# Performance work log

Hardware: AMD Instinct MI355X
Metric: run time of the kernel (lower is better)

The kernel has to match this reference:

```python
import jax, jax.numpy as jnp
import numpy as np

TEMPERATURE = 0.1
EPS = 1e-8  # torch CosineSimilarity eps


def _l2_normalize(x):
    # torch cosine sim: x / max(||x||, eps)
    n = jnp.sqrt(jnp.sum(x * x, axis=1, keepdims=True))
    return x / jnp.maximum(n, EPS)


def _pairwise_softmax(zx, zy):
    # cosine similarity matrix [N, N]: sim[i, j] = cos(zx[i], zy[j])
    sim = _l2_normalize(zx) @ _l2_normalize(zy).T  # [N, N]
    # softmax over dim=1 (columns) after temperature scaling
    return jax.nn.softmax(sim / TEMPERATURE, axis=1)


def _kl_div_mean(log_p, q):
    # torch F.kl_div(input=log_p, target=q, reduction='mean'):
    # mean over ALL elements of q * (log(q) - log_p)
    return jnp.mean(q * (jnp.log(q) - log_p))


def setup_inputs() -> dict:
    key = jax.random.key(0)
    k1, k2, k3, k4 = jax.random.split(key, 4)
    N, D = 4096, 768
    return {
        "zxs": jax.random.normal(k1, (N, D), dtype=jnp.float32),
        "zys": jax.random.normal(k2, (N, D), dtype=jnp.float32),
        "zxt": jax.random.normal(k3, (N, D), dtype=jnp.float32),
        "zyt": jax.random.normal(k4, (N, D), dtype=jnp.float32),
    }


def reference(zxs, zys, zxt, zyt):
    sim_s = _pairwise_softmax(zxs, zys)  # [N, N]
    sim_t = _pairwise_softmax(zxt, zyt)  # [N, N]
    loss_s = _kl_div_mean(jnp.log(sim_s), jax.lax.stop_gradient(sim_t))
    loss_t = _kl_div_mean(jnp.log(sim_t), jax.lax.stop_gradient(sim_s))
    return (loss_s, loss_t)
```

## Files before the change

### kernel.cpp

```cpp
#include <hip/hip_runtime.h>
#include <hip/hip_bf16.h>

#define N 4096
#define D 768
#define NC 6

typedef float f32x4 __attribute__((ext_vector_type(4)));
typedef int v8i __attribute__((ext_vector_type(8)));

typedef __attribute__((address_space(3))) unsigned int as3_uint;
typedef const __attribute__((address_space(1))) unsigned int as1_uint;

__device__ __forceinline__ void gload16(const void* g, void* l) {
    __builtin_amdgcn_global_load_lds((as1_uint*)g, (as3_uint*)l, 16, 0, 0);
}


__global__ __launch_bounds__(256) void norm4(const float* __restrict__ x0,
                                             const float* __restrict__ x1,
                                             const float* __restrict__ x2,
                                             const float* __restrict__ x3,
                                             unsigned char* __restrict__ o) {
    int a = blockIdx.y;
    const float* x = (a == 0) ? x0 : (a == 1) ? x1 : (a == 2) ? x2 : x3;
    unsigned char* out = o + (size_t)a * N * D;
    int i0 = blockIdx.x * 32;
    __shared__ __align__(16) unsigned char tile[24576];
    int t = threadIdx.x, lane = t & 63, w = t >> 6;

    for (int rr = 0; rr < 8; ++rr) {
        int R = i0 + w * 8 + rr;
        const f32x4* xr = (const f32x4*)(x + (size_t)R * D);
        f32x4 v0 = xr[lane * 2], v1 = xr[lane * 2 + 1];
        f32x4 v2 = {}, v3 = {};
        if (lane < 32) { v2 = xr[128 + lane * 2]; v3 = xr[128 + lane * 2 + 1]; }
        float ss = v0[0]*v0[0] + v0[1]*v0[1] + v0[2]*v0[2] + v0[3]*v0[3]
                 + v1[0]*v1[0] + v1[1]*v1[1] + v1[2]*v1[2] + v1[3]*v1[3]
                 + v2[0]*v2[0] + v2[1]*v2[1] + v2[2]*v2[2] + v2[3]*v2[3]
                 + v3[0]*v3[0] + v3[1]*v3[1] + v3[2]*v3[2] + v3[3]*v3[3];
        #pragma unroll
        for (int m = 1; m < 64; m <<= 1) ss += __shfl_xor(ss, m);
        float s = 1.0f / fmaxf(sqrtf(ss), 1e-8f);

        int lrg = (R >> 4) & 1;
        {
            unsigned int wlo = __builtin_amdgcn_cvt_pk_fp8_f32(v0[0]*s, v0[1]*s, 0, false) & 0xffff;
            unsigned int whi = __builtin_amdgcn_cvt_pk_fp8_f32(v0[2]*s, v0[3]*s, 0, false) & 0xffff;
            unsigned int w0 = wlo | (whi << 16);
            wlo = __builtin_amdgcn_cvt_pk_fp8_f32(v1[0]*s, v1[1]*s, 0, false) & 0xffff;
            whi = __builtin_amdgcn_cvt_pk_fp8_f32(v1[2]*s, v1[3]*s, 0, false) & 0xffff;
            unsigned int w1 = wlo | (whi << 16);
            int g = lane;
            int off = (lrg * 6 + (g >> 4)) * 2048 + ((g >> 1) & 1) * 1024
                    + ((R & 15) + 16 * ((g & 15) >> 2)) * 16 + (g & 1) * 8;
            *(uint2*)(tile + off) = make_uint2(w0, w1);
        }
        if (lane < 32) {
            unsigned int wlo = __builtin_amdgcn_cvt_pk_fp8_f32(v2[0]*s, v2[1]*s, 0, false) & 0xffff;
            unsigned int whi = __builtin_amdgcn_cvt_pk_fp8_f32(v2[2]*s, v2[3]*s, 0, false) & 0xffff;
            unsigned int w0 = wlo | (whi << 16);
            wlo = __builtin_amdgcn_cvt_pk_fp8_f32(v3[0]*s, v3[1]*s, 0, false) & 0xffff;
            whi = __builtin_amdgcn_cvt_pk_fp8_f32(v3[2]*s, v3[3]*s, 0, false) & 0xffff;
            unsigned int w1 = wlo | (whi << 16);
            int g = 64 + lane;
            int off = (lrg * 6 + (g >> 4)) * 2048 + ((g >> 1) & 1) * 1024
                    + ((R & 15) + 16 * ((g & 15) >> 2)) * 16 + (g & 1) * 8;
            *(uint2*)(tile + off) = make_uint2(w0, w1);
        }
    }
    __syncthreads();
    unsigned char* dst = out + (size_t)(i0 >> 5) * 24576;
    #pragma unroll
    for (int i = 0; i < 6; ++i)
        ((int4*)dst)[t + i * 256] = ((const int4*)tile)[t + i * 256];
}

__device__ __forceinline__ void gemm_pass(const unsigned char* __restrict__ A,
                                          const unsigned char* __restrict__ B,
                                          char* smem, int ib, int jb, int t,
                                          f32x4 (&acc)[4][4]) {
    const int lane = t & 63, w = t >> 6;
    const int wm = w >> 1, wn = w & 1;

    const unsigned char* gA = A + (size_t)((ib * 8 + 2 * w) * 6) * 2048 + lane * 16;
    const unsigned char* gB = B + (size_t)((jb * 8 + 2 * w) * 6) * 2048 + lane * 16;
    char* cur = smem;
    char* nxt = smem + 32768;
    const int sd = w * 4096 + lane * 16;

    #define ISSUE(dst, c)  do {                                                  \
        const unsigned char* _a = gA + (c) * 2048;                               \
        gload16(_a,         (dst) + sd);                                         \
        gload16(_a + 1024,  (dst) + sd + 1024);                                  \
        gload16(_a + 12288, (dst) + sd + 2048);                                  \
        gload16(_a + 13312, (dst) + sd + 3072);                                  \
        const unsigned char* _b = gB + (c) * 2048;                               \
        gload16(_b,         (dst) + 16384 + sd);                                 \
        gload16(_b + 1024,  (dst) + 16384 + sd + 1024);                          \
        gload16(_b + 12288, (dst) + 16384 + sd + 2048);                          \
        gload16(_b + 13312, (dst) + 16384 + sd + 3072);                          \
    } while (0)

    ISSUE(cur, 0);

    #pragma unroll 1
    for (int c = 0; c < NC; ++c) {
        if (c < NC - 1) {
            ISSUE(nxt, c + 1);
            asm volatile("s_waitcnt vmcnt(8)" ::: "memory");
        } else {
            asm volatile("s_waitcnt vmcnt(0)" ::: "memory");
        }
        __builtin_amdgcn_s_barrier();

        v8i a[4], b[4];
        #pragma unroll
        for (int m = 0; m < 4; ++m) {
            const char* p = cur + (wm * 4 + m) * 2048 + lane * 16;
            int4 lo = *(const int4*)p;
            int4 hi = *(const int4*)(p + 1024);
            a[m] = (v8i){lo.x, lo.y, lo.z, lo.w, hi.x, hi.y, hi.z, hi.w};
        }
        #pragma unroll
        for (int n = 0; n < 4; ++n) {
            const char* p = cur + 16384 + (wn * 4 + n) * 2048 + lane * 16;
            int4 lo = *(const int4*)p;
            int4 hi = *(const int4*)(p + 1024);
            b[n] = (v8i){lo.x, lo.y, lo.z, lo.w, hi.x, hi.y, hi.z, hi.w};
        }
        __builtin_amdgcn_s_setprio(1);
        #pragma unroll
        for (int m = 0; m < 4; ++m)
            #pragma unroll
            for (int n = 0; n < 4; ++n)
                acc[m][n] = __builtin_amdgcn_mfma_scale_f32_16x16x128_f8f6f4(
                    a[m], b[n], acc[m][n], 0, 0, 0, 127, 0, 127);
        __builtin_amdgcn_s_setprio(0);
        __builtin_amdgcn_s_barrier();
        char* tmp = cur; cur = nxt; nxt = tmp;
    }
    #undef ISSUE
}

__global__ __launch_bounds__(256, 2) void fused_gemm(
        const unsigned char* __restrict__ Xs, const unsigned char* __restrict__ Ys,
        const unsigned char* __restrict__ Xt, const unsigned char* __restrict__ Yt,
        float* __restrict__ partial) {
    __shared__ __align__(16) char smem[65536];
    const int t = threadIdx.x;
    const int jb = blockIdx.x, ib = blockIdx.y;
    const int i0 = ib * 128;
    const int lane = t & 63, wid = t >> 6;
    const int wm = wid >> 1, wn = wid & 1;

    f32x4 acc_s[4][4] = {};
    f32x4 acc_t[4][4] = {};

    gemm_pass(Xs, Ys, smem, ib, jb, t, acc_s);
    gemm_pass(Xt, Yt, smem, ib, jb, t, acc_t);

    __syncthreads();
    float* part = (float*)smem;
    int g = lane >> 4, cl = lane & 15;

    #pragma unroll
    for (int m = 0; m < 4; ++m) {
        float st[4][4];
        #pragma unroll
        for (int r = 0; r < 4; ++r) { st[r][0] = 0.f; st[r][1] = 0.f; st[r][2] = 0.f; st[r][3] = 0.f; }
        #pragma unroll
        for (int n = 0; n < 4; ++n)
            #pragma unroll
            for (int r = 0; r < 4; ++r) {
                float ls = 10.0f * acc_s[m][n][r];
                float lt = 10.0f * acc_t[m][n][r];
                float es = __expf(ls - 10.0f);
                float et = __expf(lt - 10.0f);
                st[r][0] += es;
                st[r][1] += et;
                st[r][2] += es * (ls - lt);
                st[r][3] += et * (lt - ls);
            }
        #pragma unroll
        for (int r = 0; r < 4; ++r)
            #pragma unroll
            for (int s = 0; s < 4; ++s) {
                float v = st[r][s];
                v += __shfl_xor(v, 1);
                v += __shfl_xor(v, 2);
                v += __shfl_xor(v, 4);
                v += __shfl_xor(v, 8);
                st[r][s] = v;
            }
        if (cl == 0) {
            int row = wm * 64 + m * 16 + g * 4;
            #pragma unroll
            for (int r = 0; r < 4; ++r)
                #pragma unroll
                for (int s = 0; s < 4; ++s)
                    part[(wn * 128 + row + r) * 4 + s] = st[r][s];
        }
    }
    __syncthreads();
    #pragma unroll
    for (int q = 0; q < 2; ++q) {
        int idx = t + q * 256;
        int row = idx >> 2, s = idx & 3;
        float v = part[(0 * 128 + row) * 4 + s] + part[(1 * 128 + row) * 4 + s];
        partial[((size_t)jb * N + (i0 + row)) * 4 + s] = v;
    }
}

__global__ __launch_bounds__(256) void reduce_rows(const float* __restrict__ partial,
                                                   float* __restrict__ blocksum) {
    int row = blockIdx.x * 256 + threadIdx.x;
    float zs = 0.f, zt = 0.f, ws = 0.f, wt = 0.f;
    for (int jb = 0; jb < 32; ++jb) {
        const float* p = partial + ((size_t)jb * N + row) * 4;
        zs += p[0]; zt += p[1]; ws += p[2]; wt += p[3];
    }
    float ls_row = wt / zt - logf(zt) + logf(zs);
    float lt_row = ws / zs - logf(zs) + logf(zt);
    #pragma unroll
    for (int m = 1; m < 64; m <<= 1) {
        ls_row += __shfl_xor(ls_row, m);
        lt_row += __shfl_xor(lt_row, m);
    }
    __shared__ float rs[4], rt[4];
    int lane = threadIdx.x & 63, wid = threadIdx.x >> 6;
    if (lane == 0) { rs[wid] = ls_row; rt[wid] = lt_row; }
    __syncthreads();
    if (threadIdx.x == 0) {
        blocksum[blockIdx.x * 2]     = rs[0] + rs[1] + rs[2] + rs[3];
        blocksum[blockIdx.x * 2 + 1] = rt[0] + rt[1] + rt[2] + rt[3];
    }
}

__global__ void final_reduce(const float* __restrict__ blocksum, float* __restrict__ out) {
    float a = 0.f, b = 0.f;
    if (threadIdx.x < 16) { a = blocksum[threadIdx.x * 2]; b = blocksum[threadIdx.x * 2 + 1]; }
    #pragma unroll
    for (int m = 1; m < 16; m <<= 1) { a += __shfl_xor(a, m); b += __shfl_xor(b, m); }
    if (threadIdx.x == 0) {
        const float inv = 1.0f / 16777216.0f;
        out[0] = a * inv;
        out[1] = b * inv;
    }
}

extern "C" void kernel_launch(void* const* d_in, const int* in_sizes, int n_in,
                              void* d_out, int out_size, void* d_ws, size_t ws_size,
                              hipStream_t stream) {
    const float* zxs = (const float*)d_in[0];
    const float* zys = (const float*)d_in[1];
    const float* zxt = (const float*)d_in[2];
    const float* zyt = (const float*)d_in[3];

    char* ws = (char*)d_ws;
    const size_t A = (size_t)N * D;
    unsigned char* nb = (unsigned char*)ws;
    float* partial  = (float*)(ws + 4 * A);
    float* blocksum = (float*)(ws + 4 * A + (size_t)32 * N * 4 * sizeof(float));

    norm4<<<dim3(N / 32, 4), 256, 0, stream>>>(zxs, zys, zxt, zyt, nb);

    const unsigned char* Xs = nb;
    const unsigned char* Ys = nb + A;
    const unsigned char* Xt = nb + 2 * A;
    const unsigned char* Yt = nb + 3 * A;
    fused_gemm<<<dim3(32, 32), 256, 0, stream>>>(Xs, Ys, Xt, Yt, partial);

    reduce_rows<<<16, 256, 0, stream>>>(partial, blocksum);
    final_reduce<<<1, 64, 0, stream>>>(blocksum, (float*)d_out);
}
```

Before: 61.72 us.

## Load A fragments directly from global into registers, stage only B in LDS

The A operand is now read from global memory straight into registers, with each wave loading its own four row fragments, while only B is double-buffered through LDS. The chunk loop is fully unrolled with explicit vmcnt waits. This halves shared memory use, which may allow more blocks per CU, and cuts LDS traffic for A. In exchange, waves that share rows load the same A data redundantly, and global-load latency now sits directly in front of the MFMAs instead of being hidden by prefetch.

```diff
diff --git a/kernel.cpp b/kernel.cpp
--- a/kernel.cpp
+++ b/kernel.cpp
@@ -77,76 +77,68 @@
 
 __device__ __forceinline__ void gemm_pass(const unsigned char* __restrict__ A,
                                           const unsigned char* __restrict__ B,
-                                          char* smem, int ib, int jb, int t,
+                                          char* bsm, int ib, int jb, int t,
                                           f32x4 (&acc)[4][4]) {
     const int lane = t & 63, w = t >> 6;
     const int wm = w >> 1, wn = w & 1;
 
-    const unsigned char* gA = A + (size_t)((ib * 8 + 2 * w) * 6) * 2048 + lane * 16;
+    const unsigned char* gA = A + (size_t)((ib * 8 + wm * 4) * 6) * 2048 + lane * 16;
     const unsigned char* gB = B + (size_t)((jb * 8 + 2 * w) * 6) * 2048 + lane * 16;
-    char* cur = smem;
-    char* nxt = smem + 32768;
     const int sd = w * 4096 + lane * 16;
-
-    #define ISSUE(dst, c)  do {                                                  \
-        const unsigned char* _a = gA + (c) * 2048;                               \
-        gload16(_a,         (dst) + sd);                                         \
-        gload16(_a + 1024,  (dst) + sd + 1024);                                  \
-        gload16(_a + 12288, (dst) + sd + 2048);                                  \
-        gload16(_a + 13312, (dst) + sd + 3072);                                  \
-        const unsigned char* _b = gB + (c) * 2048;                               \
-        gload16(_b,         (dst) + 16384 + sd);                                 \
-        gload16(_b + 1024,  (dst) + 16384 + sd + 1024);                          \
-        gload16(_b + 12288, (dst) + 16384 + sd + 2048);                          \
-        gload16(_b + 13312, (dst) + 16384 + sd + 3072);                          \
+    const int offB = wn * 8192 + lane * 16;
+
+    #define BSTAGE(c) do {                                                     \
+        char* d = bsm + ((c) & 1) * 16384 + sd;                                \
+        const unsigned char* s = gB + (c) * 2048;                              \
+        gload16(s,         d);                                                 \
+        gload16(s + 1024,  d + 1024);                                          \
+        gload16(s + 12288, d + 2048);                                          \
+        gload16(s + 13312, d + 3072);                                          \
     } while (0)
 
-    ISSUE(cur, 0);
-
-    #pragma unroll 1
-    for (int c = 0; c < NC; ++c) {
-        if (c < NC - 1) {
-            ISSUE(nxt, c + 1);
-            asm volatile("s_waitcnt vmcnt(8)" ::: "memory");
-        } else {
-            asm volatile("s_waitcnt vmcnt(0)" ::: "memory");
-        }
-        __builtin_amdgcn_s_barrier();
-
-        v8i a[4], b[4];
-        #pragma unroll
-        for (int m = 0; m < 4; ++m) {
-            const char* p = cur + (wm * 4 + m) * 2048 + lane * 16;
-            int4 lo = *(const int4*)p;
-            int4 hi = *(const int4*)(p + 1024);
-            a[m] = (v8i){lo.x, lo.y, lo.z, lo.w, hi.x, hi.y, hi.z, hi.w};
-        }
-        #pragma unroll
-        for (int n = 0; n < 4; ++n) {
-            const char* p = cur + 16384 + (wn * 4 + n) * 2048 + lane * 16;
-            int4 lo = *(const int4*)p;
-            int4 hi = *(const int4*)(p + 1024);
-            b[n] = (v8i){lo.x, lo.y, lo.z, lo.w, hi.x, hi.y, hi.z, hi.w};
-        }
-        __builtin_amdgcn_s_setprio(1);
-        #pragma unroll
-        for (int m = 0; m < 4; ++m)
-            #pragma unroll
-            for (int n = 0; n < 4; ++n)
-                acc[m][n] = __builtin_amdgcn_mfma_scale_f32_16x16x128_f8f6f4(
-                    a[m], b[n], acc[m][n], 0, 0, 0, 127, 0, 127);
-        __builtin_amdgcn_s_setprio(0);
-        __builtin_amdgcn_s_barrier();
-        char* tmp = cur; cur = nxt; nxt = tmp;
-    }
-    #undef ISSUE
+    BSTAGE(0);
+
+    #define CHUNK(c, VM) do {                                                  \
+        union { int4 q[2]; v8i v; } a[4];                                      \
+        _Pragma("unroll")                                                      \
+        for (int m = 0; m < 4; ++m) {                                          \
+            const unsigned char* p = gA + (size_t)m * 12288 + (c) * 2048;      \
+            a[m].q[0] = *(const int4*)p;                                       \
+            a[m].q[1] = *(const int4*)(p + 1024);                              \
+        }                                                                      \
+        if ((c) < NC - 1) BSTAGE((c) + 1);                                     \
+        asm volatile("s_waitcnt vmcnt(" #VM ")" ::: "memory");                 \
+        __builtin_amdgcn_s_barrier();                                          \
+        asm volatile("" ::: "memory");                                         \
+        const char* cb = bsm + ((c) & 1) * 16384 + offB;                       \
+        union { int4 q[2]; v8i v; } b[4];                                      \
+        _Pragma("unroll")                                                      \
+        for (int n = 0; n < 4; ++n) {                                          \
+            b[n].q[0] = *(const int4*)(cb + n * 2048);                         \
+            b[n].q[1] = *(const int4*)(cb + n * 2048 + 1024);                  \
+        }                                                                      \
+        __builtin_amdgcn_s_setprio(1);                                         \
+        _Pragma("unroll")                                                      \
+        for (int m = 0; m < 4; ++m)                                            \
+            _Pragma("unroll")                                                  \
+            for (int n = 0; n < 4; ++n)                                        \
+                acc[m][n] = __builtin_amdgcn_mfma_scale_f32_16x16x128_f8f6f4(  \
+                    a[m].v, b[n].v, acc[m][n], 0, 0, 0, 127, 0, 127);          \
+        __builtin_amdgcn_s_setprio(0);                                         \
+        __builtin_amdgcn_s_barrier();                                          \
+    } while (0)
+
+    CHUNK(0, 12); CHUNK(1, 12); CHUNK(2, 12);
+    CHUNK(3, 12); CHUNK(4, 12); CHUNK(5, 8);
+    #undef CHUNK
+    #undef BSTAGE
 }
 
 __global__ __launch_bounds__(256, 2) void fused_gemm(
         const unsigned char* __restrict__ Xs, const unsigned char* __restrict__ Ys,
         const unsigned char* __restrict__ Xt, const unsigned char* __restrict__ Yt,
         float* __restrict__ partial) {
-    __shared__ __align__(16) char smem[65536];
+    __shared__ __align__(16) char smem[32768];
     const int t = threadIdx.x;
     const int jb = blockIdx.x, ib = blockIdx.y;
     const int i0 = ib * 128;
```

After: 80.87 us. +31.0%, slower.

## Drop LDS double buffering to halve shared memory and raise occupancy

Applied to the files above, without the earlier changes.

Replaces the double-buffered prefetch pipeline in the FP8 GEMM pass with a single 32KB LDS buffer that is loaded, waited on, and consumed each chunk. Shared memory drops from 64KB to 32KB and launch bounds go from 2 to 4 blocks per CU, relying on more resident waves to hide global load latency instead of explicit prefetch. Fragment assembly now goes through a union rather than building vectors element by element. The risk is exposed load latency within each block and tighter register limits (acc_s and acc_t together take 128 VGPRs) at 4 blocks of 256 threads, which could cause spills.

```diff
diff --git a/kernel.cpp b/kernel.cpp
--- a/kernel.cpp
+++ b/kernel.cpp
@@ -84,49 +84,37 @@
 
     const unsigned char* gA = A + (size_t)((ib * 8 + 2 * w) * 6) * 2048 + lane * 16;
     const unsigned char* gB = B + (size_t)((jb * 8 + 2 * w) * 6) * 2048 + lane * 16;
-    char* cur = smem;
-    char* nxt = smem + 32768;
     const int sd = w * 4096 + lane * 16;
-
-    #define ISSUE(dst, c)  do {                                                  \
-        const unsigned char* _a = gA + (c) * 2048;                               \
-        gload16(_a,         (dst) + sd);                                         \
-        gload16(_a + 1024,  (dst) + sd + 1024);                                  \
-        gload16(_a + 12288, (dst) + sd + 2048);                                  \
-        gload16(_a + 13312, (dst) + sd + 3072);                                  \
-        const unsigned char* _b = gB + (c) * 2048;                               \
-        gload16(_b,         (dst) + 16384 + sd);                                 \
-        gload16(_b + 1024,  (dst) + 16384 + sd + 1024);                          \
-        gload16(_b + 12288, (dst) + 16384 + sd + 2048);                          \
-        gload16(_b + 13312, (dst) + 16384 + sd + 3072);                          \
-    } while (0)
-
-    ISSUE(cur, 0);
 
     #pragma unroll 1
     for (int c = 0; c < NC; ++c) {
-        if (c < NC - 1) {
-            ISSUE(nxt, c + 1);
-            asm volatile("s_waitcnt vmcnt(8)" ::: "memory");
-        } else {
-            asm volatile("s_waitcnt vmcnt(0)" ::: "memory");
-        }
+        const unsigned char* sa = gA + c * 2048;
+        const unsigned char* sb = gB + c * 2048;
+        gload16(sa,         smem + sd);
+        gload16(sa + 1024,  smem + sd + 1024);
+        gload16(sa + 12288, smem + sd + 2048);
+        gload16(sa + 13312, smem + sd + 3072);
+        gload16(sb,         smem + 16384 + sd);
+        gload16(sb + 1024,  smem + 16384 + sd + 1024);
+        gload16(sb + 12288, smem + 16384 + sd + 2048);
+        gload16(sb + 13312, smem + 16384 + sd + 3072);
+
+        asm volatile("s_waitcnt vmcnt(0)" ::: "memory");
         __builtin_amdgcn_s_barrier();
-
-        v8i a[4], b[4];
+        asm volatile("" ::: "memory");
+
+        union { int4 q[2]; v8i v; } a[4], b[4];
         #pragma unroll
         for (int m = 0; m < 4; ++m) {
-            const char* p = cur + (wm * 4 + m) * 2048 + lane * 16;
-            int4 lo = *(const int4*)p;
-            int4 hi = *(const int4*)(p + 1024);
-            a[m] = (v8i){lo.x, lo.y, lo.z, lo.w, hi.x, hi.y, hi.z, hi.w};
+            const char* p = smem + (wm * 4 + m) * 2048 + lane * 16;
+            a[m].q[0] = *(const int4*)p;
+            a[m].q[1] = *(const int4*)(p + 1024);
         }
         #pragma unroll
         for (int n = 0; n < 4; ++n) {
-            const char* p = cur + 16384 + (wn * 4 + n) * 2048 + lane * 16;
-            int4 lo = *(const int4*)p;
-            int4 hi = *(const int4*)(p + 1024);
-            b[n] = (v8i){lo.x, lo.y, lo.z, lo.w, hi.x, hi.y, hi.z, hi.w};
+            const char* p = smem + 16384 + (wn * 4 + n) * 2048 + lane * 16;
+            b[n].q[0] = *(const int4*)p;
+            b[n].q[1] = *(const int4*)(p + 1024);
         }
         __builtin_amdgcn_s_setprio(1);
         #pragma unroll
@@ -134,19 +122,17 @@
             #pragma unroll
             for (int n = 0; n < 4; ++n)
                 acc[m][n] = __builtin_amdgcn_mfma_scale_f32_16x16x128_f8f6f4(
-                    a[m], b[n], acc[m][n], 0, 0, 0, 127, 0, 127);
+                    a[m].v, b[n].v, acc[m][n], 0, 0, 0, 127, 0, 127);
         __builtin_amdgcn_s_setprio(0);
         __builtin_amdgcn_s_barrier();
-        char* tmp = cur; cur = nxt; nxt = tmp;
-    }
-    #undef ISSUE
-}
-
-__global__ __launch_bounds__(256, 2) void fused_gemm(
+    }
+}
+
+__global__ __launch_bounds__(256, 4) void fused_gemm(
         const unsigned char* __restrict__ Xs, const unsigned char* __restrict__ Ys,
         const unsigned char* __restrict__ Xt, const unsigned char* __restrict__ Yt,
         float* __restrict__ partial) {
-    __shared__ __align__(16) char smem[65536];
+    __shared__ __align__(16) char smem[32768];
     const int t = threadIdx.x;
     const int jb = blockIdx.x, ib = blockIdx.y;
     const int i0 = ib * 128;
```

Result: slower. 97.02 us (+57.2%).
